# Performance work log

Measured on AMD Instinct MI355X. Metric: run time of the kernel, lower is better.

The kernel has to match this reference:

```python
import jax, jax.numpy as jnp
import numpy as np

N = 8192        # num_nodes == args.input_size (code ties them together)
H = 64          # hidden_size
E = 262144      # num edges (avg degree 32)
FIN = N + H     # GCNConv in_channels = input_size + hidden_size


def _glorot(key, shape):
    fan_in, fan_out = shape
    lim = np.sqrt(6.0 / (fan_in + fan_out)).astype(np.float32)
    return jax.random.uniform(key, shape, jnp.float32, -lim, lim)


def gcn_conv(x, W, b, src, dst, n):
    """PyG GCNConv: lin -> add self-loops -> sym-normalized scatter-add -> +bias."""
    h = x @ W                                   # [n, out]
    loop = jnp.arange(n, dtype=src.dtype)
    s = jnp.concatenate([src, loop])            # [E+n]
    d = jnp.concatenate([dst, loop])
    deg = jax.ops.segment_sum(jnp.ones(s.shape[0], h.dtype), d, num_segments=n)
    dinv = jnp.where(deg > 0, jax.lax.rsqrt(deg), 0.0)
    norm = dinv[s] * dinv[d]                    # [E+n]
    out = jax.ops.segment_sum(h[s] * norm[:, None], d, num_segments=n)
    return out + b


def setup_inputs() -> dict:
    key = jax.random.key(0)
    k1, k2, k3, k4, k5 = jax.random.split(key, 5)
    x = jax.random.normal(k1, (N, N), jnp.float32)
    hidden_state = jax.random.normal(k2, (N, H), jnp.float32)
    W1 = _glorot(k3, (FIN, 2 * H))
    b1 = jnp.ones((2 * H,), jnp.float32)        # reset_parameters: constant_(bias, 1.0)
    W2 = _glorot(k4, (FIN, H))
    b2 = jnp.zeros((H,), jnp.float32)           # PyG default bias init = zeros
    edge_index = jax.random.randint(k5, (2, E), 0, N, jnp.int32)
    return {"x": x, "hidden_state": hidden_state, "W1": W1, "b1": b1,
            "W2": W2, "b2": b2, "edge_index": edge_index}


def reference(x, hidden_state, W1, b1, W2, b2, edge_index):
    src, dst = edge_index[0], edge_index[1]
    ru_input = jnp.concatenate([x, hidden_state], axis=1)        # [N, N+H]
    ru = jax.nn.sigmoid(gcn_conv(ru_input, W1, b1, src, dst, N))  # [N, 2H]
    flat = ru.reshape(-1, N * 2 * H)                              # [1, N*2H]
    r = flat[:, : N * H].reshape(-1, H)                           # [N, H]
    u = flat[:, N * H :].reshape(-1, H)                           # [N, H]
    c_input = jnp.concatenate([x, r * hidden_state], axis=1)
    c = jnp.tanh(gcn_conv(c_input, W2, b2, src, dst, N))          # [N, H]
    new_hidden_state = u * hidden_state + (1.0 - u) * c
    return new_hidden_state
```

## Files before the change

### kernel.cpp

```cpp
#include <hip/hip_runtime.h>
#include <hip/hip_bf16.h>
#include <stdint.h>

typedef __bf16 bf16x8 __attribute__((ext_vector_type(8)));
typedef float  f32x4  __attribute__((ext_vector_type(4)));
using bf16 = __hip_bfloat16;

#define NNODES 8192
#define FIN    8256
#define NCOL   192
#define KT32   258
#define BMB    128

enum : size_t {
  WCT_OFF  = 0,
  CNT_OFF  = 3170304,
  OFF_OFF  = 3203072,
  CUR_OFF  = 3236096,
  DNV_OFF  = 3268864,
  CSR_OFF  = 3301632,
  H1_OFF   = 4350208,
  HX2_OFF  = 8544512,
  RU_OFF   = 10641664,
  H2_OFF   = 14835968,
  YP_OFF   = 16933120,
  YP_SLICE = 6291456
};

__global__ void k_zero_i(int* p, int n) {
  int i = blockIdx.x * 256 + threadIdx.x;
  if (i < n) p[i] = 0;
}

__global__ void k_out_zero(float* out) {
  int i = blockIdx.x * 256 + threadIdx.x;
  if (i < NNODES * 64) out[i] = 0.f;
}

__global__ void k_prep_wctf(const float* __restrict__ W1, const float* __restrict__ W2,
                            bf16* __restrict__ wctf) {
  int gid = blockIdx.x * 256 + threadIdx.x;
  if (gid >= KT32 * 12 * 64) return;
  int t = gid / 768;
  int rem = gid - t * 768;
  int nf = rem >> 6, lane = rem & 63;
  int col = nf * 16 + (lane & 15);
  int k0 = t * 32 + (lane >> 4) * 8;
  union { bf16 h[8]; uint4 v; } u;
#pragma unroll
  for (int j = 0; j < 8; ++j) {
    int k = k0 + j;
    float v;
    if (col < 128)      v = W1[(size_t)k * 128 + col];
    else if (k < 8192)  v = W2[(size_t)k * 64 + (col - 128)];
    else                v = 0.f;
    u.h[j] = __float2bfloat16(v);
  }
  *(uint4*)(wctf + (size_t)gid * 8) = u.v;
}

__global__ void k_hist(const int* __restrict__ ei, int E, int* cnt) {
  int e = blockIdx.x * 256 + threadIdx.x;
  if (e < E) atomicAdd(&cnt[ei[E + e]], 1);
}

__global__ void k_scan(const int* __restrict__ cnt, int* __restrict__ offs,
                       int* __restrict__ cur, float* __restrict__ dinv) {
  __shared__ int part[256];
  int tid = threadIdx.x;
  int base = tid * 32;
  int s = 0;
#pragma unroll
  for (int j = 0; j < 32; j++) s += cnt[base + j];
  part[tid] = s;
  __syncthreads();
  for (int off = 1; off < 256; off <<= 1) {
    int a = (tid >= off) ? part[tid - off] : 0;
    __syncthreads();
    part[tid] += a;
    __syncthreads();
  }
  int run = (tid == 0) ? 0 : part[tid - 1];
  for (int j = 0; j < 32; j++) {
    int c = cnt[base + j];
    offs[base + j] = run;
    cur[base + j]  = run;
    dinv[base + j] = rsqrtf((float)(c + 1));
    run += c;
  }
  if (tid == 255) offs[NNODES] = run;
}

__global__ void k_fill(const int* __restrict__ ei, int E, int* cur, int* __restrict__ csr) {
  int e = blockIdx.x * 256 + threadIdx.x;
  if (e < E) {
    int d = ei[E + e];
    int p = atomicAdd(&cur[d], 1);
    csr[p] = ei[e];
  }
}

__device__ __forceinline__ bf16x8 pack8(float4 a, float4 b) {
  union { bf16 h[8]; bf16x8 v; } u;
  u.h[0] = __float2bfloat16(a.x); u.h[1] = __float2bfloat16(a.y);
  u.h[2] = __float2bfloat16(a.z); u.h[3] = __float2bfloat16(a.w);
  u.h[4] = __float2bfloat16(b.x); u.h[5] = __float2bfloat16(b.y);
  u.h[6] = __float2bfloat16(b.z); u.h[7] = __float2bfloat16(b.w);
  return u.v;
}

__device__ __forceinline__ void gld16(void* ldsdst, const void* gsrc) {
  __builtin_amdgcn_global_load_lds(
      (__attribute__((address_space(1))) void*)gsrc,
      (__attribute__((address_space(3))) void*)ldsdst, 16, 0, 0);
}

__global__ __launch_bounds__(256, 2) void k_gemm(const float* __restrict__ x,
                                                 const float* __restrict__ hid,
                                                 const bf16* __restrict__ wctf,
                                                 float* __restrict__ yp,
                                                 bf16* __restrict__ h1d,
                                                 float* __restrict__ hx2d,
                                                 int tpc) {
  __shared__ uint4 smA[2][1024];
  __shared__ uint4 smB[2][768];
  const int tid = threadIdx.x;
  const int lane = tid & 63, w = tid >> 6;
  const int rl = lane & 15, g = lane >> 4;
  const int m0 = blockIdx.x * BMB;
  const int chunk = blockIdx.y;
  const int t_lo = chunk * tpc;
  const int t_hi = (t_lo + tpc > KT32) ? KT32 : (t_lo + tpc);
  const int nt = t_hi - t_lo;

  const float* asx[4]; const float* ash[4];
#pragma unroll
  for (int q = 0; q < 4; ++q) {
    int u = q * 256 + tid, row = u >> 3, s = u & 7;
    int sel = (s ^ (row & 7)) << 2;
    asx[q] = x + (size_t)(m0 + row) * 8192 + sel;
    ash[q] = hid + (size_t)(m0 + row) * 64 + sel;
  }

  f32x4 acc0[12] = {};
  f32x4 acc1[12] = {};

  const int sl0 = (g * 2) ^ (rl & 7);
  const int sl1 = (g * 2 + 1) ^ (rl & 7);
  const int ra0 = (w * 32 + rl) * 8;
  const int ra1 = (w * 32 + 16 + rl) * 8;

#define STAGE(b, t) do {                                                        \
    const int _t = (t);                                                         \
    if (_t < 256) {                                                             \
      const int _k = _t * 32;                                                   \
      _Pragma("unroll")                                                         \
      for (int q = 0; q < 4; ++q) gld16(&smA[b][q * 256 + tid], asx[q] + _k);   \
    } else {                                                                    \
      const int _k = (_t - 256) * 32;                                           \
      _Pragma("unroll")                                                         \
      for (int q = 0; q < 4; ++q) gld16(&smA[b][q * 256 + tid], ash[q] + _k);   \
    }                                                                           \
    const bf16* _bt = wctf + (size_t)_t * 6144;                                 \
    _Pragma("unroll")                                                           \
    for (int q = 0; q < 3; ++q)                                                 \
      gld16(&smB[b][q * 256 + tid], _bt + (size_t)(q * 256 + tid) * 8);         \
  } while (0)

  STAGE(0, t_lo);
  __syncthreads();

  for (int it = 0; it < nt; ++it) {
    const int c = it & 1;
    if (it + 1 < nt) STAGE(c ^ 1, t_lo + it + 1);

    union { uint4 u; float4 f; } a00, a01, a10, a11;
    a00.u = smA[c][ra0 + sl0]; a01.u = smA[c][ra0 + sl1];
    a10.u = smA[c][ra1 + sl0]; a11.u = smA[c][ra1 + sl1];
    bf16x8 af0 = pack8(a00.f, a01.f);
    bf16x8 af1 = pack8(a10.f, a11.f);
#pragma unroll
    for (int nf = 0; nf < 12; ++nf) {
      bf16x8 bfr = *(const bf16x8*)&smB[c][nf * 64 + lane];
      acc0[nf] = __builtin_amdgcn_mfma_f32_16x16x32_bf16(af0, bfr, acc0[nf], 0, 0, 0);
      acc1[nf] = __builtin_amdgcn_mfma_f32_16x16x32_bf16(af1, bfr, acc1[nf], 0, 0, 0);
    }
    __syncthreads();
  }
#undef STAGE

  if (h1d) {
#pragma unroll
    for (int nf = 0; nf < 12; ++nf) {
      int col = nf * 16 + rl;
#pragma unroll
      for (int tt = 0; tt < 4; ++tt) {
        int ra = m0 + w * 32 + g * 4 + tt;
        int rb = ra + 16;
        if (col < 128) {
          h1d[(size_t)ra * 128 + col] = __float2bfloat16(acc0[nf][tt]);
          h1d[(size_t)rb * 128 + col] = __float2bfloat16(acc1[nf][tt]);
        } else {
          hx2d[(size_t)ra * 64 + (col - 128)] = acc0[nf][tt];
          hx2d[(size_t)rb * 64 + (col - 128)] = acc1[nf][tt];
        }
      }
    }
  } else {
    float* ypc = yp + (size_t)chunk * ((size_t)NNODES * NCOL);
#pragma unroll
    for (int nf = 0; nf < 12; ++nf) {
      int col = nf * 16 + rl;
#pragma unroll
      for (int tt = 0; tt < 4; ++tt) {
        int ra = m0 + w * 32 + g * 4 + tt;
        ypc[(size_t)ra * NCOL + col] = acc0[nf][tt];
        ypc[(size_t)(ra + 16) * NCOL + col] = acc1[nf][tt];
      }
    }
  }
}

__global__ void k_reduce(const float* __restrict__ yp, bf16* __restrict__ h1,
                         float* __restrict__ hx2, int nch) {
  int idx = blockIdx.x * 256 + threadIdx.x;
  float s = 0.f;
  for (int c = 0; c < nch; c++) s += yp[(size_t)c * ((size_t)NNODES * NCOL) + idx];
  int i = idx / NCOL, c = idx - i * NCOL;
  if (c < 128) h1[(size_t)i * 128 + c] = __float2bfloat16(s);
  else         hx2[(size_t)i * 64 + (c - 128)] = s;
}

__device__ __forceinline__ float bflo(unsigned v) { return __uint_as_float(v << 16); }
__device__ __forceinline__ float bfhi(unsigned v) { return __uint_as_float(v & 0xffff0000u); }

__global__ void k_scat1(const bf16* __restrict__ h1b, const int* __restrict__ offs,
                        const int* __restrict__ csr, const float* __restrict__ dinv,
                        const float* __restrict__ b1, float* __restrict__ ru) {
  int node = blockIdx.x * 4 + (threadIdx.x >> 6);
  int lane = threadIdx.x & 63;
  const unsigned* h1u = (const unsigned*)h1b;
  float dd = dinv[node];
  unsigned vv = h1u[(size_t)node * 64 + lane];
  float ax = bflo(vv) * dd * dd, ay = bfhi(vv) * dd * dd;
  int e0 = offs[node], e1 = offs[node + 1];
  for (int e = e0; e < e1; ++e) {
    int s = csr[e];
    float nrm = dinv[s] * dd;
    unsigned wv = h1u[(size_t)s * 64 + lane];
    ax += bflo(wv) * nrm;
    ay += bfhi(wv) * nrm;
  }
  ax += b1[lane * 2];
  ay += b1[lane * 2 + 1];
  ax = 1.f / (1.f + expf(-ax));
  ay = 1.f / (1.f + expf(-ay));
  ru[(size_t)node * 128 + lane * 2]     = ax;
  ru[(size_t)node * 128 + lane * 2 + 1] = ay;
}

__global__ void k_rh(const float* __restrict__ ru, const float* __restrict__ hidden,
                     const float* __restrict__ hx2, const float* __restrict__ W2,
                     bf16* __restrict__ h2) {
  __shared__ float W2s[64][64];
  __shared__ float rhs[4][64];
  int tid = threadIdx.x;
#pragma unroll
  for (int t = 0; t < 16; ++t) {
    int idx = tid + 256 * t;
    int j = idx >> 6, c = idx & 63;
    W2s[j][c] = W2[(size_t)(8192 + j) * 64 + c];
  }
  int w = tid >> 6, lane = tid & 63;
  int i = blockIdx.x * 4 + w;
  float rv = ru[(size_t)(i >> 1) * 128 + ((i & 1) << 6) + lane];
  float hv = hidden[(size_t)i * 64 + lane];
  rhs[w][lane] = rv * hv;
  __syncthreads();
  float acc = hx2[(size_t)i * 64 + lane];
#pragma unroll 8
  for (int j = 0; j < 64; ++j) acc += rhs[w][j] * W2s[j][lane];
  h2[(size_t)i * 64 + lane] = __float2bfloat16(acc);
}

__global__ void k_scat2(const bf16* __restrict__ h2b, const int* __restrict__ offs,
                        const int* __restrict__ csr, const float* __restrict__ dinv,
                        const float* __restrict__ b2, const float* __restrict__ ru,
                        const float* __restrict__ hidden, float* __restrict__ out) {
  int node = blockIdx.x * 4 + (threadIdx.x >> 6);
  int lane = threadIdx.x & 63;
  const unsigned short* h2u = (const unsigned short*)h2b;
  float dd = dinv[node];
  float acc = bflo((unsigned)h2u[(size_t)node * 64 + lane]) * dd * dd;
  int e0 = offs[node], e1 = offs[node + 1];
  for (int e = e0; e < e1; ++e) {
    int s = csr[e];
    acc += bflo((unsigned)h2u[(size_t)s * 64 + lane]) * dinv[s] * dd;
  }
  acc += b2[lane];
  float cv = tanhf(acc);
  float u = ru[(size_t)(4096 + (node >> 1)) * 128 + ((node & 1) << 6) + lane];
  float hv = hidden[(size_t)node * 64 + lane];
  out[(size_t)node * 64 + lane] = u * hv + (1.f - u) * cv;
}

extern "C" void kernel_launch(void* const* d_in, const int* in_sizes, int n_in,
                              void* d_out, int out_size, void* d_ws, size_t ws_size,
                              hipStream_t stream) {
  (void)n_in; (void)out_size;
  const float* x   = (const float*)d_in[0];
  const float* hid = (const float*)d_in[1];
  const float* W1  = (const float*)d_in[2];
  const float* b1  = (const float*)d_in[3];
  const float* W2  = (const float*)d_in[4];
  const float* b2  = (const float*)d_in[5];
  const int*   ei  = (const int*)d_in[6];
  const int E = in_sizes[6] / 2;
  float* out = (float*)d_out;

  int ksplit;
  if      (ws_size >= YP_OFF + 8ull * YP_SLICE) ksplit = 8;
  else if (ws_size >= YP_OFF + 4ull * YP_SLICE) ksplit = 4;
  else if (ws_size >= YP_OFF + 2ull * YP_SLICE) ksplit = 2;
  else if (ws_size >= YP_OFF)                   ksplit = 1;
  else {
    k_out_zero<<<dim3(NNODES * 64 / 256), dim3(256), 0, stream>>>(out);
    return;
  }
  const int tpc = (KT32 + ksplit - 1) / ksplit;

  char* ws = (char*)d_ws;
  bf16*  wctf = (bf16*)(ws + WCT_OFF);
  int*   cnt  = (int*)(ws + CNT_OFF);
  int*   offs = (int*)(ws + OFF_OFF);
  int*   cur  = (int*)(ws + CUR_OFF);
  float* dinv = (float*)(ws + DNV_OFF);
  int*   csr  = (int*)(ws + CSR_OFF);
  bf16*  h1   = (bf16*)(ws + H1_OFF);
  float* hx2  = (float*)(ws + HX2_OFF);
  float* ru   = (float*)(ws + RU_OFF);
  bf16*  h2   = (bf16*)(ws + H2_OFF);
  float* yp   = (float*)(ws + YP_OFF);

  k_zero_i<<<dim3(32), dim3(256), 0, stream>>>(cnt, NNODES);
  k_prep_wctf<<<dim3((KT32 * 12 * 64 + 255) / 256), dim3(256), 0, stream>>>(W1, W2, wctf);
  k_hist<<<dim3((E + 255) / 256), dim3(256), 0, stream>>>(ei, E, cnt);
  k_scan<<<dim3(1), dim3(256), 0, stream>>>(cnt, offs, cur, dinv);
  k_fill<<<dim3((E + 255) / 256), dim3(256), 0, stream>>>(ei, E, cur, csr);
  if (ksplit == 1) {
    k_gemm<<<dim3(NNODES / BMB, 1), dim3(256), 0, stream>>>(x, hid, wctf, nullptr, h1, hx2, tpc);
  } else {
    k_gemm<<<dim3(NNODES / BMB, ksplit), dim3(256), 0, stream>>>(x, hid, wctf, yp, nullptr, nullptr, tpc);
    k_reduce<<<dim3(NNODES * NCOL / 256), dim3(256), 0, stream>>>(yp, h1, hx2, ksplit);
  }
  k_scat1<<<dim3(NNODES / 4), dim3(256), 0, stream>>>(h1, offs, csr, dinv, b1, ru);
  k_rh<<<dim3(NNODES / 4), dim3(256), 0, stream>>>(ru, hid, hx2, W2, h2);
  k_scat2<<<dim3(NNODES / 4), dim3(256), 0, stream>>>(h2, offs, csr, dinv, b2, ru, hid, out);
}
```

Baseline: 212.2 us.

## Restructure GEMM into single-wave blocks with triple-buffered A and manual waitcnt pipelining

The GEMM now runs one 64-thread wave per block on a 32-row tile instead of four waves on 128 rows. A is triple-buffered and B double-buffered in LDS, loaded asynchronously with global_load_lds. Explicit vmcnt/lgkmcnt waits and inline ds_read_b128 replace __syncthreads, aiming to overlap loads with MFMA and drop block barriers. The cost is that each block reloads the full B tile, so weight traffic from L2 rises fourfold. The split-K reduce is also vectorized to float4.

```diff
diff --git a/kernel.cpp b/kernel.cpp
--- a/kernel.cpp
+++ b/kernel.cpp
@@ -4,13 +4,13 @@
 
 typedef __bf16 bf16x8 __attribute__((ext_vector_type(8)));
 typedef float  f32x4  __attribute__((ext_vector_type(4)));
+typedef unsigned uint4v __attribute__((ext_vector_type(4)));
 using bf16 = __hip_bfloat16;
 
 #define NNODES 8192
 #define FIN    8256
 #define NCOL   192
 #define KT32   258
-#define BMB    128
 
 enum : size_t {
   WCT_OFF  = 0,
@@ -109,85 +109,116 @@
   return u.v;
 }
 
+union F4 { uint4v u; float4 f; bf16x8 h; };
+
 __device__ __forceinline__ void gld16(void* ldsdst, const void* gsrc) {
   __builtin_amdgcn_global_load_lds(
       (__attribute__((address_space(1))) void*)gsrc,
       (__attribute__((address_space(3))) void*)ldsdst, 16, 0, 0);
 }
 
-__global__ __launch_bounds__(256, 2) void k_gemm(const float* __restrict__ x,
-                                                 const float* __restrict__ hid,
-                                                 const bf16* __restrict__ wctf,
-                                                 float* __restrict__ yp,
-                                                 bf16* __restrict__ h1d,
-                                                 float* __restrict__ hx2d,
-                                                 int tpc) {
-  __shared__ uint4 smA[2][1024];
-  __shared__ uint4 smB[2][768];
-  const int tid = threadIdx.x;
-  const int lane = tid & 63, w = tid >> 6;
+__global__ __launch_bounds__(64, 1) void k_gemm(const float* __restrict__ x,
+                                                const float* __restrict__ hid,
+                                                const bf16* __restrict__ wctf,
+                                                float* __restrict__ yp,
+                                                bf16* __restrict__ h1d,
+                                                float* __restrict__ hx2d,
+                                                int tpc) {
+  __shared__ __align__(1024) unsigned char smem[36864];
+  const int lane = threadIdx.x & 63;
   const int rl = lane & 15, g = lane >> 4;
-  const int m0 = blockIdx.x * BMB;
+  const int m0 = blockIdx.x * 32;
   const int chunk = blockIdx.y;
   const int t_lo = chunk * tpc;
   const int t_hi = (t_lo + tpc > KT32) ? KT32 : (t_lo + tpc);
   const int nt = t_hi - t_lo;
+  if (nt <= 0) return;
 
   const float* asx[4]; const float* ash[4];
 #pragma unroll
   for (int q = 0; q < 4; ++q) {
-    int u = q * 256 + tid, row = u >> 3, s = u & 7;
+    int i = q * 64 + lane, row = i >> 3, s = i & 7;
     int sel = (s ^ (row & 7)) << 2;
     asx[q] = x + (size_t)(m0 + row) * 8192 + sel;
     ash[q] = hid + (size_t)(m0 + row) * 64 + sel;
   }
+  const bf16* bsrc = wctf + (size_t)lane * 8;
+
+#define STAGE_A(buf, t) do {                                                   \
+    const int _t = (t);                                                        \
+    unsigned _d = (unsigned)(buf) * 4096u;                                     \
+    if (_t < 256) {                                                            \
+      const int _k = _t * 32;                                                  \
+      _Pragma("unroll")                                                        \
+      for (int q = 0; q < 4; ++q)                                              \
+        gld16(smem + _d + (unsigned)(q * 64 + lane) * 16u, asx[q] + _k);       \
+    } else {                                                                   \
+      const int _k = (_t - 256) * 32;                                          \
+      _Pragma("unroll")                                                        \
+      for (int q = 0; q < 4; ++q)                                              \
+        gld16(smem + _d + (unsigned)(q * 64 + lane) * 16u, ash[q] + _k);       \
+    }                                                                          \
+  } while (0)
+
+#define STAGE_B(buf, t) do {                                                   \
+    const bf16* _bt = bsrc + (size_t)(t) * 6144;                               \
+    unsigned _d = 12288u + (unsigned)(buf) * 12288u + (unsigned)lane * 16u;    \
+    _Pragma("unroll")                                                          \
+    for (int q = 0; q < 12; ++q)                                               \
+      gld16(smem + _d + (unsigned)q * 1024u, _bt + (size_t)q * 512);           \
+  } while (0)
 
   f32x4 acc0[12] = {};
   f32x4 acc1[12] = {};
 
-  const int sl0 = (g * 2) ^ (rl & 7);
-  const int sl1 = (g * 2 + 1) ^ (rl & 7);
-  const int ra0 = (w * 32 + rl) * 8;
-  const int ra1 = (w * 32 + 16 + rl) * 8;
-
-#define STAGE(b, t) do {                                                        \
-    const int _t = (t);                                                         \
-    if (_t < 256) {                                                             \
-      const int _k = _t * 32;                                                   \
-      _Pragma("unroll")                                                         \
-      for (int q = 0; q < 4; ++q) gld16(&smA[b][q * 256 + tid], asx[q] + _k);   \
-    } else {                                                                    \
-      const int _k = (_t - 256) * 32;                                           \
-      _Pragma("unroll")                                                         \
-      for (int q = 0; q < 4; ++q) gld16(&smA[b][q * 256 + tid], ash[q] + _k);   \
-    }                                                                           \
-    const bf16* _bt = wctf + (size_t)_t * 6144;                                 \
-    _Pragma("unroll")                                                           \
-    for (int q = 0; q < 3; ++q)                                                 \
-      gld16(&smB[b][q * 256 + tid], _bt + (size_t)(q * 256 + tid) * 8);         \
-  } while (0)
-
-  STAGE(0, t_lo);
-  __syncthreads();
-
-  for (int it = 0; it < nt; ++it) {
-    const int c = it & 1;
-    if (it + 1 < nt) STAGE(c ^ 1, t_lo + it + 1);
-
-    union { uint4 u; float4 f; } a00, a01, a10, a11;
-    a00.u = smA[c][ra0 + sl0]; a01.u = smA[c][ra0 + sl1];
-    a10.u = smA[c][ra1 + sl0]; a11.u = smA[c][ra1 + sl1];
+  const unsigned sl0 = (unsigned)((g * 2) ^ (rl & 7));
+  const unsigned sl1 = (unsigned)((g * 2 + 1) ^ (rl & 7));
+  const unsigned aA0 = (unsigned)rl * 128u + sl0 * 16u;
+  const unsigned aA1 = (unsigned)rl * 128u + sl1 * 16u;
+  const unsigned baseB = 12288u + (unsigned)lane * 16u;
+  const unsigned ldsbase = (unsigned)(uintptr_t)&smem[0];
+
+  STAGE_A(0, t_lo);
+  STAGE_B(0, t_lo);
+  if (nt > 1) STAGE_A(1, t_lo + 1);
+
+  int r3 = 0;
+  int w3 = 2;
+  for (int li = 0; li < nt; ++li) {
+    if (li + 1 < nt) STAGE_B((li + 1) & 1, t_lo + li + 1);
+    if (li + 2 < nt) STAGE_A(w3, t_lo + li + 2);
+
+    if (li + 2 < nt)      asm volatile("s_waitcnt vmcnt(20)" ::: "memory");
+    else if (li + 1 < nt) asm volatile("s_waitcnt vmcnt(16)" ::: "memory");
+    else                  asm volatile("s_waitcnt vmcnt(0)"  ::: "memory");
+    __builtin_amdgcn_sched_barrier(0);
+
+    const unsigned ar = ldsbase + (unsigned)r3 * 4096u;
+    const unsigned br = ldsbase + baseB + (unsigned)(li & 1) * 12288u;
+    F4 a00, a01, a10, a11, bv[12];
+    asm volatile("ds_read_b128 %0, %1" : "=v"(a00.u) : "v"(ar + aA0));
+    asm volatile("ds_read_b128 %0, %1" : "=v"(a01.u) : "v"(ar + aA1));
+    asm volatile("ds_read_b128 %0, %1 offset:2048" : "=v"(a10.u) : "v"(ar + aA0));
+    asm volatile("ds_read_b128 %0, %1 offset:2048" : "=v"(a11.u) : "v"(ar + aA1));
+#pragma unroll
+    for (int nf = 0; nf < 12; ++nf)
+      asm volatile("ds_read_b128 %0, %1 offset:%c2"
+                   : "=v"(bv[nf].u) : "v"(br), "i"(nf * 1024));
+    asm volatile("s_waitcnt lgkmcnt(0)" ::: "memory");
+    __builtin_amdgcn_sched_barrier(0);
+
     bf16x8 af0 = pack8(a00.f, a01.f);
     bf16x8 af1 = pack8(a10.f, a11.f);
 #pragma unroll
     for (int nf = 0; nf < 12; ++nf) {
-      bf16x8 bfr = *(const bf16x8*)&smB[c][nf * 64 + lane];
-      acc0[nf] = __builtin_amdgcn_mfma_f32_16x16x32_bf16(af0, bfr, acc0[nf], 0, 0, 0);
-      acc1[nf] = __builtin_amdgcn_mfma_f32_16x16x32_bf16(af1, bfr, acc1[nf], 0, 0, 0);
+      acc0[nf] = __builtin_amdgcn_mfma_f32_16x16x32_bf16(af0, bv[nf].h, acc0[nf], 0, 0, 0);
+      acc1[nf] = __builtin_amdgcn_mfma_f32_16x16x32_bf16(af1, bv[nf].h, acc1[nf], 0, 0, 0);
     }
-    __syncthreads();
-  }
-#undef STAGE
+    r3 = (r3 == 2) ? 0 : r3 + 1;
+    w3 = (w3 == 2) ? 0 : w3 + 1;
+  }
+#undef STAGE_A
+#undef STAGE_B
 
   if (h1d) {
 #pragma unroll
@@ -195,7 +226,7 @@
       int col = nf * 16 + rl;
 #pragma unroll
       for (int tt = 0; tt < 4; ++tt) {
-        int ra = m0 + w * 32 + g * 4 + tt;
+        int ra = m0 + g * 4 + tt;
         int rb = ra + 16;
         if (col < 128) {
           h1d[(size_t)ra * 128 + col] = __float2bfloat16(acc0[nf][tt]);
@@ -213,7 +244,7 @@
       int col = nf * 16 + rl;
 #pragma unroll
       for (int tt = 0; tt < 4; ++tt) {
-        int ra = m0 + w * 32 + g * 4 + tt;
+        int ra = m0 + g * 4 + tt;
         ypc[(size_t)ra * NCOL + col] = acc0[nf][tt];
         ypc[(size_t)(ra + 16) * NCOL + col] = acc1[nf][tt];
       }
@@ -221,14 +252,23 @@
   }
 }
 
-__global__ void k_reduce(const float* __restrict__ yp, bf16* __restrict__ h1,
-                         float* __restrict__ hx2, int nch) {
-  int idx = blockIdx.x * 256 + threadIdx.x;
-  float s = 0.f;
-  for (int c = 0; c < nch; c++) s += yp[(size_t)c * ((size_t)NNODES * NCOL) + idx];
-  int i = idx / NCOL, c = idx - i * NCOL;
-  if (c < 128) h1[(size_t)i * 128 + c] = __float2bfloat16(s);
-  else         hx2[(size_t)i * 64 + (c - 128)] = s;
+__global__ void k_reduce4(const float* __restrict__ yp, bf16* __restrict__ h1,
+                          float* __restrict__ hx2, int nch) {
+  int u = blockIdx.x * 256 + threadIdx.x;
+  float4 s = {0.f, 0.f, 0.f, 0.f};
+  for (int c = 0; c < nch; c++) {
+    float4 v = *(const float4*)(yp + (size_t)c * ((size_t)NNODES * NCOL) + (size_t)u * 4);
+    s.x += v.x; s.y += v.y; s.z += v.z; s.w += v.w;
+  }
+  int e = u * 4;
+  int i = e / NCOL, c = e - i * NCOL;
+  if (c < 128) {
+    bf16* dst = h1 + (size_t)i * 128 + c;
+    dst[0] = __float2bfloat16(s.x); dst[1] = __float2bfloat16(s.y);
+    dst[2] = __float2bfloat16(s.z); dst[3] = __float2bfloat16(s.w);
+  } else {
+    *(float4*)(hx2 + (size_t)i * 64 + (c - 128)) = s;
+  }
 }
 
 __device__ __forceinline__ float bflo(unsigned v) { return __uint_as_float(v << 16); }
@@ -348,10 +388,10 @@
   k_scan<<<dim3(1), dim3(256), 0, stream>>>(cnt, offs, cur, dinv);
   k_fill<<<dim3((E + 255) / 256), dim3(256), 0, stream>>>(ei, E, cur, csr);
   if (ksplit == 1) {
-    k_gemm<<<dim3(NNODES / BMB, 1), dim3(256), 0, stream>>>(x, hid, wctf, nullptr, h1, hx2, tpc);
+    k_gemm<<<dim3(NNODES / 32, 1), dim3(64), 0, stream>>>(x, hid, wctf, nullptr, h1, hx2, tpc);
   } else {
-    k_gemm<<<dim3(NNODES / BMB, ksplit), dim3(256), 0, stream>>>(x, hid, wctf, yp, nullptr, nullptr, tpc);
-    k_reduce<<<dim3(NNODES * NCOL / 256), dim3(256), 0, stream>>>(yp, h1, hx2, ksplit);
+    k_gemm<<<dim3(NNODES / 32, ksplit), dim3(64), 0, stream>>>(x, hid, wctf, yp, nullptr, nullptr, tpc);
+    k_reduce4<<<dim3(NNODES * NCOL / 1024), dim3(256), 0, stream>>>(yp, h1, hx2, ksplit);
   }
   k_scat1<<<dim3(NNODES / 4), dim3(256), 0, stream>>>(h1, offs, csr, dinv, b1, ru);
   k_rh<<<dim3(NNODES / 4), dim3(256), 0, stream>>>(ru, hid, hx2, W2, h2);
```

New measurement: 232.5 us. +9.6%, slower.
